# Performance work log

Measured on AMD Instinct MI355X. Metric: run time of the kernel, lower is better.

## Reference

```python
import jax, jax.numpy as jnp
import numpy as np

B, S, H = 32, 4096, 1024


def setup_inputs() -> dict:
    key = jax.random.key(0)
    ks = jax.random.split(key, 6)
    sc = 1.0 / np.sqrt(H)
    return {
        "hidden_state": jax.random.normal(ks[0], (B, 1, H), dtype=jnp.float32),
        "encoder_outputs": jax.random.normal(ks[1], (B, S, H), dtype=jnp.float32),
        "A_w": jax.random.normal(ks[2], (H, H), dtype=jnp.float32) * sc,
        "A_b": jax.random.normal(ks[3], (H,), dtype=jnp.float32) * 0.01,
        "C_w": jax.random.normal(ks[4], (H, 2 * H), dtype=jnp.float32) * sc,
        "C_b": jax.random.normal(ks[5], (H,), dtype=jnp.float32) * 0.01,
    }


def reference(hidden_state, encoder_outputs, A_w, A_b, C_w, C_b):
    # NOTE: source applies A twice to hidden_state (first reassignment, then
    # again inside the bmm). We reproduce that exactly.
    h1 = hidden_state @ A_w.T + A_b            # [B,1,H] (reassigned hidden_state)
    h2 = h1 @ A_w.T + A_b                      # second A application for scores
    scores = jnp.einsum('bsh,bqh->bsq', encoder_outputs, h2)   # [B,S,1]
    attn = jax.nn.softmax(scores, axis=1)                      # softmax over S
    context = jnp.einsum('bsq,bsh->bqh', attn, encoder_outputs)  # [B,1,H]
    concat = jnp.concatenate([h1[:, 0], context[:, 0]], axis=1)  # [B,2H]
    out = jnp.tanh(concat @ C_w.T + C_b)                         # [B,H]
    return out, attn
```

## Files before the change

kernel.cpp:

```cpp
#include <hip/hip_runtime.h>
#include <math.h>

#define B_ 32
#define S_ 4096
#define H_ 1024

#define RPB   128
#define NBLK  (S_ / RPB)
#define RPW   32

__device__ __forceinline__ float wave_reduce_sum(float v) {
    #pragma unroll
    for (int o = 32; o > 0; o >>= 1) v += __shfl_xor(v, o, 64);
    return v;
}

__device__ __forceinline__ void wave_reduce_sum2(float& a, float& b) {
    #pragma unroll
    for (int o = 32; o > 0; o >>= 1) {
        a += __shfl_xor(a, o, 64);
        b += __shfl_xor(b, o, 64);
    }
}

__global__ __launch_bounds__(256) void gemv_aw(const float* __restrict__ x, int xstride,
                                               const float* __restrict__ W,
                                               const float* __restrict__ bias,
                                               float* __restrict__ y, int ystride) {
    int w = threadIdx.x >> 6, lane = threadIdx.x & 63;
    int gw = blockIdx.x * 4 + w;
    int b = gw >> 10, i = gw & 1023;
    const float4* xr = reinterpret_cast<const float4*>(x + (size_t)b * xstride);
    const float4* wr = reinterpret_cast<const float4*>(W + (size_t)i * H_);
    float s = 0.f;
    #pragma unroll
    for (int k = 0; k < 4; ++k) {
        float4 a = xr[lane + k * 64];
        float4 ww = wr[lane + k * 64];
        s += a.x * ww.x + a.y * ww.y + a.z * ww.z + a.w * ww.w;
    }
    s = wave_reduce_sum(s);
    if (lane == 0) y[(size_t)b * ystride + i] = s + bias[i];
}

#define LOADPAIR(d0, d1, r) do {                                                 \
    const float4* rp_ = base + (size_t)(r) * 256;                                \
    d0[0] = rp_[0]; d0[1] = rp_[64]; d0[2] = rp_[128]; d0[3] = rp_[192];         \
    const float4* rq_ = rp_ + 256;                                               \
    d1[0] = rq_[0]; d1[1] = rq_[64]; d1[2] = rq_[128]; d1[3] = rq_[192];         \
} while (0)

#define PROCESS(va, vb, lr) do {                                                 \
    float s0 = 0.f, s1 = 0.f;                                                    \
    _Pragma("unroll")                                                            \
    for (int k = 0; k < 4; ++k) {                                                \
        s0 += va[k].x * hv[k].x + va[k].y * hv[k].y + va[k].z * hv[k].z + va[k].w * hv[k].w; \
        s1 += vb[k].x * hv[k].x + vb[k].y * hv[k].y + vb[k].z * hv[k].z + vb[k].w * hv[k].w; \
    }                                                                            \
    wave_reduce_sum2(s0, s1);                                                    \
    my_score = (lane == (lr)    ) ? s0 : my_score;                               \
    my_score = (lane == (lr) + 1) ? s1 : my_score;                               \
    float tm_ = fmaxf(s0, s1);                                                   \
    if (tm_ > m) {                                       \
        float sc_ = __expf(m - tm_);          \
        l *= sc_;                                                                \
        _Pragma("unroll")                                                        \
        for (int k = 0; k < 4; ++k) {                                            \
            acc[k].x *= sc_; acc[k].y *= sc_; acc[k].z *= sc_; acc[k].w *= sc_;  \
        }                                                                        \
        m = tm_;                                                                 \
    }                                                                            \
    float p0_ = __expf(s0 - m), p1_ = __expf(s1 - m);                            \
    l += p0_ + p1_;                                                              \
    _Pragma("unroll")                                                            \
    for (int k = 0; k < 4; ++k) {                                                \
        acc[k].x += p0_ * va[k].x + p1_ * vb[k].x;                               \
        acc[k].y += p0_ * va[k].y + p1_ * vb[k].y;                               \
        acc[k].z += p0_ * va[k].z + p1_ * vb[k].z;                               \
        acc[k].w += p0_ * va[k].w + p1_ * vb[k].w;                               \
    }                                                                            \
} while (0)

__global__ __launch_bounds__(256, 2) void attn_pass1(const float* __restrict__ enc,
                                                     const float* __restrict__ h2,
                                                     float* __restrict__ scores,
                                                     float* __restrict__ partials) {
    int b   = blockIdx.x >> 5;
    int blk = blockIdx.x & (NBLK - 1);
    int w = threadIdx.x >> 6, lane = threadIdx.x & 63;

    int row0 = blk * RPB + w * RPW;
    const float4* base = reinterpret_cast<const float4*>(
        enc + (size_t)b * S_ * H_ + (size_t)row0 * H_) + lane;

    const float4* hp = reinterpret_cast<const float4*>(h2 + (size_t)b * H_);
    float4 hv[4];
    #pragma unroll
    for (int k = 0; k < 4; ++k) hv[k] = hp[lane + k * 64];

    float m = -INFINITY, l = 0.f;
    float4 acc[4];
    #pragma unroll
    for (int k = 0; k < 4; ++k) acc[k] = make_float4(0.f, 0.f, 0.f, 0.f);
    float my_score = 0.f;

    float4 A0[4], A1[4], B0[4], B1[4], C0[4], C1[4], D0[4], D1[4];
    LOADPAIR(A0, A1, 0);
    LOADPAIR(B0, B1, 2);
    LOADPAIR(C0, C1, 4);
    LOADPAIR(D0, D1, 6);

    #pragma unroll 1
    for (int t = 0; t < RPW; t += 8) {
        PROCESS(A0, A1, t);
        if (t + 8 < RPW)  LOADPAIR(A0, A1, t + 8);
        PROCESS(B0, B1, t + 2);
        if (t + 10 < RPW) LOADPAIR(B0, B1, t + 10);
        PROCESS(C0, C1, t + 4);
        if (t + 12 < RPW) LOADPAIR(C0, C1, t + 12);
        PROCESS(D0, D1, t + 6);
        if (t + 14 < RPW) LOADPAIR(D0, D1, t + 14);
    }
    if (lane < RPW) scores[(size_t)b * S_ + row0 + lane] = my_score;

    __shared__ float lds_ctx[4][H_];
    __shared__ float lds_m[4], lds_l[4];
    float4* mc = reinterpret_cast<float4*>(&lds_ctx[w][0]);
    #pragma unroll
    for (int k = 0; k < 4; ++k) mc[lane + k * 64] = acc[k];
    if (lane == 0) { lds_m[w] = m; lds_l[w] = l; }
    __syncthreads();

    float mb = fmaxf(fmaxf(lds_m[0], lds_m[1]), fmaxf(lds_m[2], lds_m[3]));
    float sc0 = __expf(lds_m[0] - mb), sc1 = __expf(lds_m[1] - mb);
    float sc2 = __expf(lds_m[2] - mb), sc3 = __expf(lds_m[3] - mb);
    float lb = lds_l[0] * sc0 + lds_l[1] * sc1 + lds_l[2] * sc2 + lds_l[3] * sc3;

    float* part = partials + ((size_t)b * NBLK + blk) * (H_ + 2);
    #pragma unroll
    for (int k2 = 0; k2 < 4; ++k2) {
        int col = threadIdx.x + k2 * 256;
        float v = lds_ctx[0][col] * sc0 + lds_ctx[1][col] * sc1 +
                  lds_ctx[2][col] * sc2 + lds_ctx[3][col] * sc3;
        part[2 + col] = v;
    }
    if (threadIdx.x == 0) { part[0] = mb; part[1] = lb; }
}

__global__ __launch_bounds__(256) void attn_reduce(const float* __restrict__ partials,
                                                   float* __restrict__ concat,
                                                   const float* __restrict__ scores,
                                                   float* __restrict__ attn_out) {
    int b = blockIdx.x >> 2;
    int q = blockIdx.x & 3;
    const float* part = partials + (size_t)b * NBLK * (H_ + 2);
    float ms[NBLK];
    float mb = -INFINITY;
    #pragma unroll
    for (int k = 0; k < NBLK; ++k) {
        ms[k] = part[(size_t)k * (H_ + 2)];
        mb = fmaxf(mb, ms[k]);
    }
    float lb = 0.f;
    float sc[NBLK];
    #pragma unroll
    for (int k = 0; k < NBLK; ++k) {
        sc[k] = __expf(ms[k] - mb);
        lb += part[(size_t)k * (H_ + 2) + 1] * sc[k];
    }
    float inv_l = 1.f / lb;
    int col = q * 256 + threadIdx.x;
    float v = 0.f;
    #pragma unroll
    for (int k = 0; k < NBLK; ++k)
        v += part[(size_t)k * (H_ + 2) + 2 + col] * sc[k];
    concat[(size_t)b * 2048 + 1024 + col] = v * inv_l;

    const float4* sp = reinterpret_cast<const float4*>(scores + (size_t)b * S_ + q * 1024);
    float4* ap = reinterpret_cast<float4*>(attn_out + (size_t)b * S_ + q * 1024);
    float4 sv = sp[threadIdx.x];
    float4 av;
    av.x = __expf(sv.x - mb) * inv_l;
    av.y = __expf(sv.y - mb) * inv_l;
    av.z = __expf(sv.z - mb) * inv_l;
    av.w = __expf(sv.w - mb) * inv_l;
    ap[threadIdx.x] = av;
}

__global__ __launch_bounds__(256) void out_gemm(const float* __restrict__ concat,
                                                const float* __restrict__ Cw,
                                                const float* __restrict__ Cb,
                                                float* __restrict__ out) {
    int w = threadIdx.x >> 6, lane = threadIdx.x & 63;
    int i = blockIdx.x;
    const float4* wr = reinterpret_cast<const float4*>(Cw + (size_t)i * 2048);
    float4 wv[8];
    #pragma unroll
    for (int k = 0; k < 8; ++k) wv[k] = wr[lane + k * 64];
    float bias = Cb[i];
    #pragma unroll
    for (int bb = 0; bb < 8; ++bb) {
        int b = w * 8 + bb;
        const float4* cr = reinterpret_cast<const float4*>(concat + (size_t)b * 2048);
        float s = 0.f;
        #pragma unroll
        for (int k = 0; k < 8; ++k) {
            float4 c = cr[lane + k * 64];
            s += c.x * wv[k].x + c.y * wv[k].y + c.z * wv[k].z + c.w * wv[k].w;
        }
        s = wave_reduce_sum(s);
        if (lane == 0) out[(size_t)b * H_ + i] = tanhf(s + bias);
    }
}

extern "C" void kernel_launch(void* const* d_in, const int* in_sizes, int n_in,
                              void* d_out, int out_size, void* d_ws, size_t ws_size,
                              hipStream_t stream) {
    const float* hs  = (const float*)d_in[0];
    const float* enc = (const float*)d_in[1];
    const float* A_w = (const float*)d_in[2];
    const float* A_b = (const float*)d_in[3];
    const float* C_w = (const float*)d_in[4];
    const float* C_b = (const float*)d_in[5];

    float* out      = (float*)d_out;
    float* attn_out = out + B_ * H_;

    float* ws       = (float*)d_ws;
    float* concat   = ws;
    float* h2       = ws + (size_t)B_ * 2048;
    float* scores   = h2 + (size_t)B_ * H_;
    float* partials = scores + (size_t)B_ * S_;

    gemv_aw<<<(B_ * H_) / 4, 256, 0, stream>>>(hs, H_, A_w, A_b, concat, 2048);
    gemv_aw<<<(B_ * H_) / 4, 256, 0, stream>>>(concat, 2048, A_w, A_b, h2, H_);
    attn_pass1<<<B_ * NBLK, 256, 0, stream>>>(enc, h2, scores, partials);
    attn_reduce<<<B_ * 4, 256, 0, stream>>>(partials, concat, scores, attn_out);
    out_gemm<<<H_, 256, 0, stream>>>(concat, C_w, C_b, out);
}
```

Baseline: 145.2 us.

## Halve attention rows per block, batch gemv rows per wave, stage reduce scales in LDS

The attention pass now handles 64 rows per block (16 per wave) with a two-stage prefetch ring and asks for 3 blocks per CU, doubling the grid to 2048 blocks. The A-weight gemv keeps x in registers and has each wave compute 8 output rows in pairs, cutting redundant x loads and launching eight times fewer blocks. The reduce kernel loads the per-block max and sum values into shared memory once instead of every thread reading all of them from global memory. The trade-off is twice as many partial context vectors to write and reduce, and less load prefetch depth per wave.

```diff
diff --git a/kernel.cpp b/kernel.cpp
--- a/kernel.cpp
+++ b/kernel.cpp
@@ -5,9 +5,9 @@
 #define S_ 4096
 #define H_ 1024
 
-#define RPB   128
+#define RPB   64
 #define NBLK  (S_ / RPB)
-#define RPW   32
+#define RPW   16
 
 __device__ __forceinline__ float wave_reduce_sum(float v) {
     #pragma unroll
@@ -29,18 +29,29 @@
                                                float* __restrict__ y, int ystride) {
     int w = threadIdx.x >> 6, lane = threadIdx.x & 63;
     int gw = blockIdx.x * 4 + w;
-    int b = gw >> 10, i = gw & 1023;
+    int b = gw >> 7;
+    int i0 = (gw & 127) << 3;
     const float4* xr = reinterpret_cast<const float4*>(x + (size_t)b * xstride);
-    const float4* wr = reinterpret_cast<const float4*>(W + (size_t)i * H_);
-    float s = 0.f;
-    #pragma unroll
-    for (int k = 0; k < 4; ++k) {
-        float4 a = xr[lane + k * 64];
-        float4 ww = wr[lane + k * 64];
-        s += a.x * ww.x + a.y * ww.y + a.z * ww.z + a.w * ww.w;
-    }
-    s = wave_reduce_sum(s);
-    if (lane == 0) y[(size_t)b * ystride + i] = s + bias[i];
+    float4 xv[4];
+    #pragma unroll
+    for (int k = 0; k < 4; ++k) xv[k] = xr[lane + k * 64];
+    #pragma unroll
+    for (int j = 0; j < 8; j += 2) {
+        const float4* w0 = reinterpret_cast<const float4*>(W + (size_t)(i0 + j) * H_);
+        const float4* w1 = reinterpret_cast<const float4*>(W + (size_t)(i0 + j + 1) * H_);
+        float s0 = 0.f, s1 = 0.f;
+        #pragma unroll
+        for (int k = 0; k < 4; ++k) {
+            float4 a = w0[lane + k * 64], c = w1[lane + k * 64];
+            s0 += a.x * xv[k].x + a.y * xv[k].y + a.z * xv[k].z + a.w * xv[k].w;
+            s1 += c.x * xv[k].x + c.y * xv[k].y + c.z * xv[k].z + c.w * xv[k].w;
+        }
+        wave_reduce_sum2(s0, s1);
+        if (lane == 0) {
+            y[(size_t)b * ystride + i0 + j]     = s0 + bias[i0 + j];
+            y[(size_t)b * ystride + i0 + j + 1] = s1 + bias[i0 + j + 1];
+        }
+    }
 }
 
 #define LOADPAIR(d0, d1, r) do {                                                 \
@@ -81,11 +92,11 @@
     }                                                                            \
 } while (0)
 
-__global__ __launch_bounds__(256, 2) void attn_pass1(const float* __restrict__ enc,
+__global__ __launch_bounds__(256, 3) void attn_pass1(const float* __restrict__ enc,
                                                      const float* __restrict__ h2,
                                                      float* __restrict__ scores,
                                                      float* __restrict__ partials) {
-    int b   = blockIdx.x >> 5;
+    int b   = blockIdx.x >> 6;
     int blk = blockIdx.x & (NBLK - 1);
     int w = threadIdx.x >> 6, lane = threadIdx.x & 63;
 
@@ -104,22 +115,16 @@
     for (int k = 0; k < 4; ++k) acc[k] = make_float4(0.f, 0.f, 0.f, 0.f);
     float my_score = 0.f;
 
-    float4 A0[4], A1[4], B0[4], B1[4], C0[4], C1[4], D0[4], D1[4];
+    float4 A0[4], A1[4], B0[4], B1[4];
     LOADPAIR(A0, A1, 0);
     LOADPAIR(B0, B1, 2);
-    LOADPAIR(C0, C1, 4);
-    LOADPAIR(D0, D1, 6);
 
     #pragma unroll 1
-    for (int t = 0; t < RPW; t += 8) {
+    for (int t = 0; t < RPW; t += 4) {
         PROCESS(A0, A1, t);
-        if (t + 8 < RPW)  LOADPAIR(A0, A1, t + 8);
+        if (t + 4 < RPW) LOADPAIR(A0, A1, t + 4);
         PROCESS(B0, B1, t + 2);
-        if (t + 10 < RPW) LOADPAIR(B0, B1, t + 10);
-        PROCESS(C0, C1, t + 4);
-        if (t + 12 < RPW) LOADPAIR(C0, C1, t + 12);
-        PROCESS(D0, D1, t + 6);
-        if (t + 14 < RPW) LOADPAIR(D0, D1, t + 14);
+        if (t + 6 < RPW) LOADPAIR(B0, B1, t + 6);
     }
     if (lane < RPW) scores[(size_t)b * S_ + row0 + lane] = my_score;
 
@@ -154,37 +159,38 @@
     int b = blockIdx.x >> 2;
     int q = blockIdx.x & 3;
     const float* part = partials + (size_t)b * NBLK * (H_ + 2);
-    float ms[NBLK];
+    __shared__ float s_m[NBLK], s_l[NBLK], s_sc[NBLK];
+    int t = threadIdx.x;
+    if (t < NBLK) {
+        s_m[t] = part[(size_t)t * (H_ + 2)];
+        s_l[t] = part[(size_t)t * (H_ + 2) + 1];
+    }
+    __syncthreads();
     float mb = -INFINITY;
     #pragma unroll
-    for (int k = 0; k < NBLK; ++k) {
-        ms[k] = part[(size_t)k * (H_ + 2)];
-        mb = fmaxf(mb, ms[k]);
-    }
+    for (int k = 0; k < NBLK; ++k) mb = fmaxf(mb, s_m[k]);
+    if (t < NBLK) s_sc[t] = __expf(s_m[t] - mb);
+    __syncthreads();
     float lb = 0.f;
-    float sc[NBLK];
-    #pragma unroll
-    for (int k = 0; k < NBLK; ++k) {
-        sc[k] = __expf(ms[k] - mb);
-        lb += part[(size_t)k * (H_ + 2) + 1] * sc[k];
-    }
+    #pragma unroll
+    for (int k = 0; k < NBLK; ++k) lb += s_l[k] * s_sc[k];
     float inv_l = 1.f / lb;
-    int col = q * 256 + threadIdx.x;
+    int col = q * 256 + t;
     float v = 0.f;
-    #pragma unroll
+    #pragma unroll 8
     for (int k = 0; k < NBLK; ++k)
-        v += part[(size_t)k * (H_ + 2) + 2 + col] * sc[k];
+        v += part[(size_t)k * (H_ + 2) + 2 + col] * s_sc[k];
     concat[(size_t)b * 2048 + 1024 + col] = v * inv_l;
 
     const float4* sp = reinterpret_cast<const float4*>(scores + (size_t)b * S_ + q * 1024);
     float4* ap = reinterpret_cast<float4*>(attn_out + (size_t)b * S_ + q * 1024);
-    float4 sv = sp[threadIdx.x];
+    float4 sv = sp[t];
     float4 av;
     av.x = __expf(sv.x - mb) * inv_l;
     av.y = __expf(sv.y - mb) * inv_l;
     av.z = __expf(sv.z - mb) * inv_l;
     av.w = __expf(sv.w - mb) * inv_l;
-    ap[threadIdx.x] = av;
+    ap[t] = av;
 }
 
 __global__ __launch_bounds__(256) void out_gemm(const float* __restrict__ concat,
@@ -232,8 +238,8 @@
     float* scores   = h2 + (size_t)B_ * H_;
     float* partials = scores + (size_t)B_ * S_;
 
-    gemv_aw<<<(B_ * H_) / 4, 256, 0, stream>>>(hs, H_, A_w, A_b, concat, 2048);
-    gemv_aw<<<(B_ * H_) / 4, 256, 0, stream>>>(concat, 2048, A_w, A_b, h2, H_);
+    gemv_aw<<<(B_ * H_) / 32, 256, 0, stream>>>(hs, H_, A_w, A_b, concat, 2048);
+    gemv_aw<<<(B_ * H_) / 32, 256, 0, stream>>>(concat, 2048, A_w, A_b, h2, H_);
     attn_pass1<<<B_ * NBLK, 256, 0, stream>>>(enc, h2, scores, partials);
     attn_reduce<<<B_ * 4, 256, 0, stream>>>(partials, concat, scores, attn_out);
     out_gemm<<<H_, 256, 0, stream>>>(concat, C_w, C_b, out);
```

New measurement: 143.9 us. Within noise of the previous version (-0.9%).
